# Kernel tuning notes

Hardware: AMD Instinct MI355X
Metric: run time of the kernel (lower is better)

The kernel has to match this reference:

```python
import jax, jax.numpy as jnp
import numpy as np
from jax import lax

N, HW = 64, 240
C0, C1, C2, C3 = 3, 32, 64, 128
HEAD = 1280


def _conv(x, w, stride, pad):
    return lax.conv_general_dilated(
        x, w, (stride, stride), [(pad, pad), (pad, pad)],
        dimension_numbers=("NCHW", "OIHW", "NCHW"))


def _cbr(x, w, alpha, beta, stride, pad, do_relu=True):
    # conv2d with pre-folded BN: y = conv(x,w)*alpha + beta, then ReLU
    y = _conv(x, w, stride, pad)
    y = y * alpha[None, :, None, None] + beta[None, :, None, None]
    return jnp.maximum(y, 0.0) if do_relu else y


def setup_inputs() -> dict:
    key = jax.random.key(0)
    ks = jax.random.split(key, 13)
    f32 = jnp.float32
    inp = {
        "x": jax.random.normal(ks[0], (N, C0, HW, HW), dtype=f32),
        # stem 3x3 s2: 3 -> 32
        "w_stem": jax.random.normal(ks[1], (C1, C0, 3, 3), dtype=f32) * 0.1,
        "a_stem": jax.random.uniform(ks[2], (C1,), dtype=f32, minval=0.5, maxval=1.5),
        "b_stem": jax.random.normal(ks[3], (C1,), dtype=f32) * 0.1,
        # mid 3x3 s2: 32 -> 64
        "w1": jax.random.normal(ks[4], (C2, C1, 3, 3), dtype=f32) * 0.05,
        "a1": jax.random.uniform(ks[5], (C2,), dtype=f32, minval=0.5, maxval=1.5),
        "b1": jax.random.normal(ks[6], (C2,), dtype=f32) * 0.1,
        # pointwise 1x1 s1: 64 -> 128
        "w2": jax.random.normal(ks[7], (C3, C2, 1, 1), dtype=f32) * 0.05,
        "a2": jax.random.uniform(ks[8], (C3,), dtype=f32, minval=0.5, maxval=1.5),
        "b2": jax.random.normal(ks[9], (C3,), dtype=f32) * 0.1,
        # head: GAP + GEMV (w2d [Cout, Cin]) + BN-fold + ReLU
        "w_head": jax.random.normal(ks[10], (HEAD, C3), dtype=f32) * 0.05,
        "a_head": jax.random.uniform(ks[11], (HEAD,), dtype=f32, minval=0.5, maxval=1.5),
        "b_head": jax.random.normal(ks[12], (HEAD,), dtype=f32) * 0.1,
    }
    return inp


def reference(x, w_stem, a_stem, b_stem, w1, a1, b1, w2, a2, b2,
              w_head, a_head, b_head):
    h = _cbr(x, w_stem, a_stem, b_stem, stride=2, pad=1)   # [N,32,120,120]
    h = _cbr(h, w1, a1, b1, stride=2, pad=1)               # [N,64,60,60]
    h = _cbr(h, w2, a2, b2, stride=1, pad=0)               # [N,128,60,60]
    # head: global average pool + GEMV + folded-BN affine + ReLU
    gap = h.mean(axis=(2, 3))                              # [N,128]
    out = jnp.einsum("nc,oc->no", gap, w_head)             # [N,1280]
    out = out * a_head[None, :] + b_head[None, :]
    return jnp.maximum(out, 0.0)
```

## Files before the change

### kernel.cpp

```cpp
#include <hip/hip_runtime.h>

#define N_    64
#define HW_   240
#define H1_   120
#define H2_   60
#define C0_   3
#define C1_   32
#define C2_   64
#define C3_   128
#define HEAD_ 1280

typedef unsigned short US;
typedef short bf16x8 __attribute__((ext_vector_type(8)));
typedef float f32x16 __attribute__((ext_vector_type(16)));

__device__ __forceinline__ US f2bf(float f) {
  union { float f; unsigned u; } v; v.f = f;
  unsigned r = v.u + 0x7FFF + ((v.u >> 16) & 1);
  return (US)(r >> 16);
}

#define H1Q_ROW 3968
#define H1Q_PL  1984

#define ZCHN   368
#define ZTOT   (64 * ZCHN * 4)
__global__ __launch_bounds__(256) void k0_prep(
    const float* __restrict__ w1, const float* __restrict__ w2,
    const float* __restrict__ w0,
    US* __restrict__ h1q, US* __restrict__ wt1, US* __restrict__ wt2,
    US* __restrict__ wt0, float* __restrict__ gap) {
  int gid = blockIdx.x * 256 + threadIdx.x;
  if (gid < ZTOT) {
    int c = gid >> 2, q = gid & 3;
    int n = c / ZCHN, cc = c % ZCHN;
    long off; int y;
    if (cc < 124)      { y = 0;   off = (long)cc * 32; }
    else if (cc < 248) { y = 121; off = (long)(cc - 124) * 32; }
    else               { y = cc - 247; off = H1Q_PL; }
    uint4 z; z.x = z.y = z.z = z.w = 0u;
    *(uint4*)(h1q + ((long)(n * 122 + y)) * H1Q_ROW + off + q * 8) = z;
  } else if (gid < ZTOT + 18432) {
    int e = gid - ZTOT;
    int oc = e / 288, ic = (e / 9) % 32, ky = (e / 3) % 3, kx = e % 3;
    wt1[((ky * 3 + kx) * 64 + oc) * 32 + ic] = f2bf(w1[e]);
  } else if (gid < ZTOT + 18432 + 8192) {
    int e = gid - (ZTOT + 18432);
    wt2[e] = f2bf(w2[e]);
  } else if (gid < ZTOT + 18432 + 8192 + 1024) {
    int e = gid - (ZTOT + 18432 + 8192);
    int oc = e >> 5, k = e & 31;
    wt0[e] = (k < 27) ? f2bf(w0[oc * 27 + k]) : (US)0;
  } else if (gid < ZTOT + 18432 + 8192 + 1024 + 8192) {
    gap[gid - (ZTOT + 18432 + 8192 + 1024)] = 0.f;
  }
}

#define XSW 248
__global__ __launch_bounds__(256) void k1_mfma(
    const float* __restrict__ x, const US* __restrict__ wt0,
    const float* __restrict__ alpha, const float* __restrict__ beta,
    US* __restrict__ h1q) {
  __shared__ float xs[3 * 3 * XSW];
  __shared__ US ot[128 * 32];
  int y = blockIdx.x, n = blockIdx.y;
  int iy0 = 2 * y - 1;
  const float* xn = x + (long)n * C0_ * HW_ * HW_;
  for (int e = threadIdx.x; e < 540; e += 256) {
    int m = e % 60, seg = e / 60;
    int ic = seg / 3, r = seg % 3;
    int iy = iy0 + r;
    float4 v; v.x = v.y = v.z = v.w = 0.f;
    if (iy >= 0) v = *(const float4*)(xn + (long)ic * HW_ * HW_ + iy * HW_ + 4 * m);
    *(float4*)(xs + seg * XSW + 4 + 4 * m) = v;
  }
  if (threadIdx.x < 18) {
    int seg = threadIdx.x >> 1, end = threadIdx.x & 1;
    float4 z; z.x = z.y = z.z = z.w = 0.f;
    *(float4*)(xs + seg * XSW + (end ? 244 : 0)) = z;
  }
  __syncthreads();

  int t = threadIdx.x, wv = t >> 6, l = t & 63;
  int lane31 = l & 31, half = l >> 5;
  int ox = wv * 32 + lane31;
  int oxc = ox < H1_ ? ox : (H1_ - 1);

  float fa[16];
#pragma unroll
  for (int m = 0; m < 2; m++)
#pragma unroll
    for (int j = 0; j < 8; j++) {
      int k = m * 16 + half * 8 + j;
      float v = 0.f;
      if (k < 27) {
        int ic = k / 9, rem = k - ic * 9;
        int ky = rem / 3, kx = rem - ky * 3;
        v = xs[(ic * 3 + ky) * XSW + 3 + 2 * oxc + kx];
      }
      fa[m * 8 + j] = v;
    }
  bf16x8 a0, a1;
#pragma unroll
  for (int j = 0; j < 8; j++) {
    a0[j] = (short)f2bf(fa[j]);
    a1[j] = (short)f2bf(fa[8 + j]);
  }
  const US* wb = wt0 + lane31 * 32 + half * 8;
  bf16x8 b0 = *(const bf16x8*)(wb);
  bf16x8 b1 = *(const bf16x8*)(wb + 16);

  f32x16 acc;
#pragma unroll
  for (int i = 0; i < 16; i++) acc[i] = 0.f;
  acc = __builtin_amdgcn_mfma_f32_32x32x16_bf16(a0, b0, acc, 0, 0, 0);
  acc = __builtin_amdgcn_mfma_f32_32x32x16_bf16(a1, b1, acc, 0, 0, 0);

  int oc = lane31;
  float al = alpha[oc], be = beta[oc];
#pragma unroll
  for (int r = 0; r < 16; r++) {
    int row = (r & 3) + 8 * (r >> 2) + 4 * half;
    float v = fmaxf(fmaf(acc[r], al, be), 0.f);
    ot[(wv * 32 + row) * 32 + oc] = f2bf(v);
  }
  __syncthreads();

  long rowb = ((long)(n * 122 + y + 1)) * H1Q_ROW;
  for (int u = t; u < 480; u += 256) {
    int px = u >> 2, q = u & 3;
    int pl = px & 1;
    int m = (px + 1) >> 1;
    long addr = rowb + (pl ? H1Q_PL : 0) + (long)m * 32 + q * 8;
    *(uint4*)(h1q + addr) = *(const uint4*)(ot + px * 32 + q * 8);
  }
}

#define TS 72
__device__ __forceinline__ void gld_lds16(const void* g, void* l) {
  __builtin_amdgcn_global_load_lds(
      (const __attribute__((address_space(1))) unsigned int*)g,
      (__attribute__((address_space(3))) unsigned int*)l, 16, 0, 0);
}

__global__ __launch_bounds__(256, 2) void k2_fused(
    const US* __restrict__ h1q, const US* __restrict__ wt1,
    const US* __restrict__ wt2,
    const float* __restrict__ a1, const float* __restrict__ b1,
    const float* __restrict__ a2, const float* __restrict__ b2,
    float* __restrict__ gap) {
  __shared__ __align__(16) US st[6 * 4096];
  __shared__ __align__(16) US tile[64 * TS];
  int t = threadIdx.x, w = t >> 6, l = t & 63;
  int lane31 = l & 31, half = l >> 5;

  int n = 8 * blockIdx.x + (blockIdx.y & 7);
  int bxr = blockIdx.y >> 3;
  int ny = bxr < 4 ? 8 : 7;
  int y0 = bxr < 4 ? bxr * 8 : 32 + (bxr - 4) * 7;

  const char* nb = (const char*)(h1q + (long)(n * 122) * H1Q_ROW);

  int wm = w & 1, wn = w >> 1;
  int oc = wn * 32 + lane31;
  int pt = w & 1, og = w >> 1;
  bf16x8 wA[9][2];
#pragma unroll
  for (int kk = 0; kk < 9; kk++)
#pragma unroll
    for (int c = 0; c < 2; c++)
      wA[kk][c] = *(const bf16x8*)(wt1 + (kk * 64 + oc) * 32 + half * 8 + c * 16);
  bf16x8 wB[2][4];
  float al2[2], be2[2];
#pragma unroll
  for (int nt = 0; nt < 2; nt++) {
    int oc2 = (og * 2 + nt) * 32 + lane31;
#pragma unroll
    for (int c = 0; c < 4; c++)
      wB[nt][c] = *(const bf16x8*)(wt2 + oc2 * 64 + half * 8 + c * 16);
    al2[nt] = a2[oc2]; be2[nt] = b2[oc2];
  }
  float al1 = a1[oc], be1 = b1[oc];

  int px = wm * 32 + lane31;
  int xx = px < 60 ? px : 59;
  int abase = xx * 32 + half * 8;
  int usofs[3][2];
#pragma unroll
  for (int kx = 0; kx < 3; kx++)
#pragma unroll
    for (int c = 0; c < 2; c++) {
      int uo = (kx == 1 ? 0 : (kx == 0 ? 1984 : 2016)) + abase + c * 16;
      usofs[kx][c] = uo ^ (((uo >> 6) & 7) << 3);
    }

#pragma unroll
  for (int i = 0; i < 6; i++) {
    int c = i * 256 + t;
    int rw = c >> 9;
    int b = (c & 511) * 16;
    int sb = b ^ (((b >> 7) & 7) << 4);
    int r = 2 * y0 + rw;
    gld_lds16(nb + (long)r * 7936 + sb, (char*)st + (r % 6) * 8192 + b);
  }
  __syncthreads();

  for (int iy = 0; iy < ny; iy++) {
    int y = y0 + iy;
    if (iy + 1 < ny) {
#pragma unroll
      for (int i = 0; i < 4; i++) {
        int c = i * 256 + t;
        int rw = c >> 9;
        int b = (c & 511) * 16;
        int sb = b ^ (((b >> 7) & 7) << 4);
        int r = 2 * y + 3 + rw;
        gld_lds16(nb + (long)r * 7936 + sb,
                  (char*)st + (r % 6) * 8192 + b);
      }
    }

    f32x16 acc;
#pragma unroll
    for (int i = 0; i < 16; i++) acc[i] = 0.f;
#pragma unroll
    for (int ky = 0; ky < 3; ky++) {
      int r = 2 * y + ky;
      int sb6 = (r % 6) * 4096;
#pragma unroll
      for (int kx = 0; kx < 3; kx++) {
#pragma unroll
        for (int c = 0; c < 2; c++) {
          bf16x8 av = *(const bf16x8*)(st + sb6 + usofs[kx][c]);
          acc = __builtin_amdgcn_mfma_f32_32x32x16_bf16(av, wA[ky * 3 + kx][c],
                                                        acc, 0, 0, 0);
        }
      }
    }
#pragma unroll
    for (int r = 0; r < 16; r++) {
      int row = (r & 3) + 8 * (r >> 2) + 4 * half;
      tile[(wm * 32 + row) * TS + oc] = f2bf(fmaxf(fmaf(acc[r], al1, be1), 0.f));
    }
    __syncthreads();

    const US* ab = tile + (pt * 32 + lane31) * TS + half * 8;
    bf16x8 af[4];
#pragma unroll
    for (int c = 0; c < 4; c++) af[c] = *(const bf16x8*)(ab + c * 16);

#pragma unroll
    for (int nt = 0; nt < 2; nt++) {
      int oc2 = (og * 2 + nt) * 32 + lane31;
      f32x16 acc2;
#pragma unroll
      for (int i = 0; i < 16; i++) acc2[i] = 0.f;
#pragma unroll
      for (int c = 0; c < 4; c++)
        acc2 = __builtin_amdgcn_mfma_f32_32x32x16_bf16(af[c], wB[nt][c], acc2,
                                                       0, 0, 0);
      float s = 0.f;
      if (pt == 0) {
#pragma unroll
        for (int r = 0; r < 16; r++) s += fmaxf(fmaf(acc2[r], al2[nt], be2[nt]), 0.f);
      } else {
#pragma unroll
        for (int r = 0; r < 16; r++) {
          int row = (r & 3) + 8 * (r >> 2) + 4 * half;
          if (32 + row < 60) s += fmaxf(fmaf(acc2[r], al2[nt], be2[nt]), 0.f);
        }
      }
      s += __shfl_xor(s, 32);
      if (half == 0) atomicAdd(gap + n * C3_ + oc2, s);
    }
    __syncthreads();
  }
}

__global__ __launch_bounds__(256) void k4_head(
    const float* __restrict__ gap, const float* __restrict__ wh,
    const float* __restrict__ alpha, const float* __restrict__ beta,
    float* __restrict__ out) {
  __shared__ float g[8 * C3_];
  int n0 = blockIdx.y * 8;
  int t = threadIdx.x;
  for (int e = t; e < 8 * C3_; e += 256)
    g[e] = gap[n0 * C3_ + e] * (1.f / 3600.f);
  __syncthreads();
  int o = blockIdx.x * 256 + t;
  const float* wr = wh + (long)o * C3_;
  float acc[8];
#pragma unroll
  for (int i = 0; i < 8; i++) acc[i] = 0.f;
#pragma unroll 4
  for (int c = 0; c < C3_; c += 4) {
    float4 wv = *(const float4*)(wr + c);
#pragma unroll
    for (int i = 0; i < 8; i++) {
      const float* gi = g + i * C3_ + c;
      acc[i] = fmaf(wv.x, gi[0], acc[i]);
      acc[i] = fmaf(wv.y, gi[1], acc[i]);
      acc[i] = fmaf(wv.z, gi[2], acc[i]);
      acc[i] = fmaf(wv.w, gi[3], acc[i]);
    }
  }
  float al = alpha[o], be = beta[o];
#pragma unroll
  for (int i = 0; i < 8; i++)
    out[(n0 + i) * HEAD_ + o] = fmaxf(fmaf(acc[i], al, be), 0.f);
}

extern "C" void kernel_launch(void* const* d_in, const int* in_sizes, int n_in,
                              void* d_out, int out_size, void* d_ws,
                              size_t ws_size, hipStream_t stream) {
  const float* x      = (const float*)d_in[0];
  const float* w_stem = (const float*)d_in[1];
  const float* a_stem = (const float*)d_in[2];
  const float* b_stem = (const float*)d_in[3];
  const float* w1     = (const float*)d_in[4];
  const float* a1     = (const float*)d_in[5];
  const float* b1     = (const float*)d_in[6];
  const float* w2     = (const float*)d_in[7];
  const float* a2     = (const float*)d_in[8];
  const float* b2     = (const float*)d_in[9];
  const float* wh     = (const float*)d_in[10];
  const float* ah     = (const float*)d_in[11];
  const float* bh     = (const float*)d_in[12];
  float* out = (float*)d_out;

  US* h1q = (US*)d_ws;
  US* wt1 = h1q + (size_t)N_ * 122 * H1Q_ROW;
  US* wt2 = wt1 + 9 * 64 * 32;
  US* wt0 = wt2 + C3_ * C2_;
  float* gap = (float*)(wt0 + 1024);

  {
    int total = ZTOT + 18432 + 8192 + 1024 + 8192;
    k0_prep<<<(total + 255) / 256, 256, 0, stream>>>(w1, w2, w_stem, h1q,
                                                     wt1, wt2, wt0, gap);
  }
  {
    dim3 grid(H1_, N_);
    k1_mfma<<<grid, 256, 0, stream>>>(x, wt0, a_stem, b_stem, h1q);
  }
  {
    dim3 grid(8, N_);
    k2_fused<<<grid, 256, 0, stream>>>(h1q, wt1, wt2, a1, b1, a2, b2, gap);
  }
  {
    dim3 grid(HEAD_ / 256, 8);
    k4_head<<<grid, 256, 0, stream>>>(gap, wh, ah, bh, out);
  }
}
```

Baseline: 153.0 us.

## Fuse stem convolution into the fused mid/pointwise kernel via LDS ring buffers

Removes the separate stem kernel and its bf16 intermediate buffer in global memory. Each block of the fused kernel now streams raw input rows into a 6-row LDS ring, computes the stem conv with MFMA directly into the swizzled h1 ring consumed by the 3x3 conv, and overlaps the next rows' stem work with the pointwise stage. This saves the global write and re-read of the 120x120x32 activation and one launch, and no longer needs the zero-fill of padding. In exchange, stem rows on block boundaries are recomputed, LDS use per block grows, and the stem work is serialized inside each block's row loop.

Result: slower. 167.8 us (+9.6%).

```diff
diff --git a/kernel.cpp b/kernel.cpp
--- a/kernel.cpp
+++ b/kernel.cpp
@@ -20,72 +20,43 @@
   return (US)(r >> 16);
 }
 
-#define H1Q_ROW 3968
-#define H1Q_PL  1984
-
-#define ZCHN   368
-#define ZTOT   (64 * ZCHN * 4)
 __global__ __launch_bounds__(256) void k0_prep(
     const float* __restrict__ w1, const float* __restrict__ w2,
     const float* __restrict__ w0,
-    US* __restrict__ h1q, US* __restrict__ wt1, US* __restrict__ wt2,
+    US* __restrict__ wt1, US* __restrict__ wt2,
     US* __restrict__ wt0, float* __restrict__ gap) {
   int gid = blockIdx.x * 256 + threadIdx.x;
-  if (gid < ZTOT) {
-    int c = gid >> 2, q = gid & 3;
-    int n = c / ZCHN, cc = c % ZCHN;
-    long off; int y;
-    if (cc < 124)      { y = 0;   off = (long)cc * 32; }
-    else if (cc < 248) { y = 121; off = (long)(cc - 124) * 32; }
-    else               { y = cc - 247; off = H1Q_PL; }
-    uint4 z; z.x = z.y = z.z = z.w = 0u;
-    *(uint4*)(h1q + ((long)(n * 122 + y)) * H1Q_ROW + off + q * 8) = z;
-  } else if (gid < ZTOT + 18432) {
-    int e = gid - ZTOT;
+  if (gid < 18432) {
+    int e = gid;
     int oc = e / 288, ic = (e / 9) % 32, ky = (e / 3) % 3, kx = e % 3;
     wt1[((ky * 3 + kx) * 64 + oc) * 32 + ic] = f2bf(w1[e]);
-  } else if (gid < ZTOT + 18432 + 8192) {
-    int e = gid - (ZTOT + 18432);
+  } else if (gid < 18432 + 8192) {
+    int e = gid - 18432;
     wt2[e] = f2bf(w2[e]);
-  } else if (gid < ZTOT + 18432 + 8192 + 1024) {
-    int e = gid - (ZTOT + 18432 + 8192);
+  } else if (gid < 18432 + 8192 + 1024) {
+    int e = gid - (18432 + 8192);
     int oc = e >> 5, k = e & 31;
     wt0[e] = (k < 27) ? f2bf(w0[oc * 27 + k]) : (US)0;
-  } else if (gid < ZTOT + 18432 + 8192 + 1024 + 8192) {
-    gap[gid - (ZTOT + 18432 + 8192 + 1024)] = 0.f;
-  }
-}
-
-#define XSW 248
-__global__ __launch_bounds__(256) void k1_mfma(
-    const float* __restrict__ x, const US* __restrict__ wt0,
-    const float* __restrict__ alpha, const float* __restrict__ beta,
-    US* __restrict__ h1q) {
-  __shared__ float xs[3 * 3 * XSW];
-  __shared__ US ot[128 * 32];
-  int y = blockIdx.x, n = blockIdx.y;
-  int iy0 = 2 * y - 1;
-  const float* xn = x + (long)n * C0_ * HW_ * HW_;
-  for (int e = threadIdx.x; e < 540; e += 256) {
-    int m = e % 60, seg = e / 60;
-    int ic = seg / 3, r = seg % 3;
-    int iy = iy0 + r;
-    float4 v; v.x = v.y = v.z = v.w = 0.f;
-    if (iy >= 0) v = *(const float4*)(xn + (long)ic * HW_ * HW_ + iy * HW_ + 4 * m);
-    *(float4*)(xs + seg * XSW + 4 + 4 * m) = v;
-  }
-  if (threadIdx.x < 18) {
-    int seg = threadIdx.x >> 1, end = threadIdx.x & 1;
-    float4 z; z.x = z.y = z.z = z.w = 0.f;
-    *(float4*)(xs + seg * XSW + (end ? 244 : 0)) = z;
-  }
-  __syncthreads();
-
-  int t = threadIdx.x, wv = t >> 6, l = t & 63;
-  int lane31 = l & 31, half = l >> 5;
-  int ox = wv * 32 + lane31;
-  int oxc = ox < H1_ ? ox : (H1_ - 1);
-
+  } else if (gid < 18432 + 8192 + 1024 + 8192) {
+    gap[gid - (18432 + 8192 + 1024)] = 0.f;
+  }
+}
+
+#define TS 72
+__device__ __forceinline__ void gld_lds16(const void* g, void* l) {
+  __builtin_amdgcn_global_load_lds(
+      (const __attribute__((address_space(1))) unsigned int*)g,
+      (__attribute__((address_space(3))) unsigned int*)l, 16, 0, 0);
+}
+
+__device__ __forceinline__ void stem_tile(
+    const float* xr, US* st, int gy, int tb, int lane31, int half,
+    bf16x8 sb0, bf16x8 sb1, float al0, float be0) {
+  int px = tb + lane31;
+  int oxc = px < H1_ ? px : (H1_ - 1);
+  int sl[3];
+#pragma unroll
+  for (int ky = 0; ky < 3; ky++) sl[ky] = (2 * gy - 1 + ky + 6) % 6;
   float fa[16];
 #pragma unroll
   for (int m = 0; m < 2; m++)
@@ -96,7 +67,7 @@
       if (k < 27) {
         int ic = k / 9, rem = k - ic * 9;
         int ky = rem / 3, kx = rem - ky * 3;
-        v = xs[(ic * 3 + ky) * XSW + 3 + 2 * oxc + kx];
+        v = xr[sl[ky] * 768 + ic * 256 + 3 + 2 * oxc + kx];
       }
       fa[m * 8 + j] = v;
     }
@@ -106,50 +77,34 @@
     a0[j] = (short)f2bf(fa[j]);
     a1[j] = (short)f2bf(fa[8 + j]);
   }
-  const US* wb = wt0 + lane31 * 32 + half * 8;
-  bf16x8 b0 = *(const bf16x8*)(wb);
-  bf16x8 b1 = *(const bf16x8*)(wb + 16);
-
   f32x16 acc;
 #pragma unroll
   for (int i = 0; i < 16; i++) acc[i] = 0.f;
-  acc = __builtin_amdgcn_mfma_f32_32x32x16_bf16(a0, b0, acc, 0, 0, 0);
-  acc = __builtin_amdgcn_mfma_f32_32x32x16_bf16(a1, b1, acc, 0, 0, 0);
-
-  int oc = lane31;
-  float al = alpha[oc], be = beta[oc];
+  acc = __builtin_amdgcn_mfma_f32_32x32x16_bf16(a0, sb0, acc, 0, 0, 0);
+  acc = __builtin_amdgcn_mfma_f32_32x32x16_bf16(a1, sb1, acc, 0, 0, 0);
+  int r6 = ((gy + 1) % 6) * 4096;
 #pragma unroll
   for (int r = 0; r < 16; r++) {
     int row = (r & 3) + 8 * (r >> 2) + 4 * half;
-    float v = fmaxf(fmaf(acc[r], al, be), 0.f);
-    ot[(wv * 32 + row) * 32 + oc] = f2bf(v);
-  }
-  __syncthreads();
-
-  long rowb = ((long)(n * 122 + y + 1)) * H1Q_ROW;
-  for (int u = t; u < 480; u += 256) {
-    int px = u >> 2, q = u & 3;
-    int pl = px & 1;
-    int m = (px + 1) >> 1;
-    long addr = rowb + (pl ? H1Q_PL : 0) + (long)m * 32 + q * 8;
-    *(uint4*)(h1q + addr) = *(const uint4*)(ot + px * 32 + q * 8);
-  }
-}
-
-#define TS 72
-__device__ __forceinline__ void gld_lds16(const void* g, void* l) {
-  __builtin_amdgcn_global_load_lds(
-      (const __attribute__((address_space(1))) unsigned int*)g,
-      (__attribute__((address_space(3))) unsigned int*)l, 16, 0, 0);
-}
-
-__global__ __launch_bounds__(256, 2) void k2_fused(
-    const US* __restrict__ h1q, const US* __restrict__ wt1,
-    const US* __restrict__ wt2,
+    int pxo = tb + row;
+    if (pxo < H1_) {
+      int pl = pxo & 1, mm = (pxo + 1) >> 1;
+      int uo = pl * 1984 + mm * 32 + lane31;
+      int us = uo ^ (((uo >> 6) & 7) << 3);
+      st[r6 + us] = f2bf(fmaxf(fmaf(acc[r], al0, be0), 0.f));
+    }
+  }
+}
+
+__global__ __launch_bounds__(256, 2) void k12_fused(
+    const float* __restrict__ x, const US* __restrict__ wt0,
+    const US* __restrict__ wt1, const US* __restrict__ wt2,
+    const float* __restrict__ a0p, const float* __restrict__ b0p,
     const float* __restrict__ a1, const float* __restrict__ b1,
     const float* __restrict__ a2, const float* __restrict__ b2,
     float* __restrict__ gap) {
   __shared__ __align__(16) US st[6 * 4096];
+  __shared__ __align__(16) float xr[6 * 768];
   __shared__ __align__(16) US tile[64 * TS];
   int t = threadIdx.x, w = t >> 6, l = t & 63;
   int lane31 = l & 31, half = l >> 5;
@@ -159,11 +114,15 @@
   int ny = bxr < 4 ? 8 : 7;
   int y0 = bxr < 4 ? bxr * 8 : 32 + (bxr - 4) * 7;
 
-  const char* nb = (const char*)(h1q + (long)(n * 122) * H1Q_ROW);
+  const float* xn = x + (long)n * C0_ * HW_ * HW_;
 
   int wm = w & 1, wn = w >> 1;
   int oc = wn * 32 + lane31;
   int pt = w & 1, og = w >> 1;
+  const US* wb = wt0 + lane31 * 32 + half * 8;
+  bf16x8 sb0 = *(const bf16x8*)(wb);
+  bf16x8 sb1 = *(const bf16x8*)(wb + 16);
+  float al0 = a0p[lane31], be0 = b0p[lane31];
   bf16x8 wA[9][2];
 #pragma unroll
   for (int kk = 0; kk < 9; kk++)
@@ -182,8 +141,8 @@
   }
   float al1 = a1[oc], be1 = b1[oc];
 
-  int px = wm * 32 + lane31;
-  int xx = px < 60 ? px : 59;
+  int px2 = wm * 32 + lane31;
+  int xx = px2 < 60 ? px2 : 59;
   int abase = xx * 32 + half * 8;
   int usofs[3][2];
 #pragma unroll
@@ -194,32 +153,74 @@
       usofs[kx][c] = uo ^ (((uo >> 6) & 7) << 3);
     }
 
-#pragma unroll
-  for (int i = 0; i < 6; i++) {
-    int c = i * 256 + t;
-    int rw = c >> 9;
-    int b = (c & 511) * 16;
-    int sb = b ^ (((b >> 7) & 7) << 4);
-    int r = 2 * y0 + rw;
-    gld_lds16(nb + (long)r * 7936 + sb, (char*)st + (r % 6) * 8192 + b);
-  }
-  __syncthreads();
-
-  for (int iy = 0; iy < ny; iy++) {
-    int y = y0 + iy;
-    if (iy + 1 < ny) {
-#pragma unroll
-      for (int i = 0; i < 4; i++) {
+  {
+    uint4 z; z.x = z.y = z.z = z.w = 0u;
+    for (int e = t; e < 4224; e += 256) {
+      if (e < 3072) ((uint4*)st)[e] = z;
+      else          ((uint4*)xr)[e - 3072] = z;
+    }
+  }
+  __syncthreads();
+  {
+    int r0 = 4 * y0 - 3;
+#pragma unroll
+    for (int i = 0; i < 4; i++) {
+      int c = i * 256 + t;
+      if (c < 960) {
+        int rc = c >> 6;
+        int iy = r0 + rc / 3, ic = rc - (rc / 3) * 3;
+        if (iy >= 0 && (t & 63) < 60)
+          gld_lds16((const char*)(xn + (long)ic * HW_ * HW_ + (long)iy * HW_) +
+                        (t & 63) * 16,
+                    (char*)xr + ((iy % 6) * 768 + ic * 256) * 4 + 16 +
+                        (t & 63) * 16);
+      }
+    }
+  }
+  __syncthreads();
+  for (int j = 0; j < 2; j++) {
+    int gy = 2 * y0 - 1 + j;
+    if (gy >= 0)
+      stem_tile(xr, st, gy, w * 32, lane31, half, sb0, sb1, al0, be0);
+  }
+  __syncthreads();
+  {
+    int r0 = 4 * y0 + 2;
+#pragma unroll
+    for (int i = 0; i < 2; i++) {
+      int c = i * 256 + t;
+      if (c < 384) {
+        int rc = c >> 6;
+        int iy = r0 + rc / 3, ic = rc - (rc / 3) * 3;
+        if ((t & 63) < 60)
+          gld_lds16((const char*)(xn + (long)ic * HW_ * HW_ + (long)iy * HW_) +
+                        (t & 63) * 16,
+                    (char*)xr + ((iy % 6) * 768 + ic * 256) * 4 + 16 +
+                        (t & 63) * 16);
+      }
+    }
+  }
+  __syncthreads();
+  stem_tile(xr, st, 2 * y0 + 1, w * 32, lane31, half, sb0, sb1, al0, be0);
+  __syncthreads();
+
+  for (int it = 0; it < ny; ++it) {
+    int y = y0 + it;
+    bool more = (it + 1 < ny);
+    if (more) {
+      int r0 = 4 * y + 4;
+#pragma unroll
+      for (int i = 0; i < 3; i++) {
         int c = i * 256 + t;
-        int rw = c >> 9;
-        int b = (c & 511) * 16;
-        int sb = b ^ (((b >> 7) & 7) << 4);
-        int r = 2 * y + 3 + rw;
-        gld_lds16(nb + (long)r * 7936 + sb,
-                  (char*)st + (r % 6) * 8192 + b);
-      }
-    }
-
+        int rc = c >> 6;
+        int iy = r0 + rc / 3, ic = rc - (rc / 3) * 3;
+        if ((t & 63) < 60)
+          gld_lds16((const char*)(xn + (long)ic * HW_ * HW_ + (long)iy * HW_) +
+                        (t & 63) * 16,
+                    (char*)xr + ((iy % 6) * 768 + ic * 256) * 4 + 16 +
+                        (t & 63) * 16);
+      }
+    }
     f32x16 acc;
 #pragma unroll
     for (int i = 0; i < 16; i++) acc[i] = 0.f;
@@ -244,11 +245,17 @@
     }
     __syncthreads();
 
+    if (more) {
+      int gy = 2 * y + 2 + (w >> 1);
+      int ws = w & 1;
+      stem_tile(xr, st, gy, ws * 32, lane31, half, sb0, sb1, al0, be0);
+      stem_tile(xr, st, gy, 64 + ws * 32, lane31, half, sb0, sb1, al0, be0);
+    }
+
     const US* ab = tile + (pt * 32 + lane31) * TS + half * 8;
     bf16x8 af[4];
 #pragma unroll
     for (int c = 0; c < 4; c++) af[c] = *(const bf16x8*)(ab + c * 16);
-
 #pragma unroll
     for (int nt = 0; nt < 2; nt++) {
       int oc2 = (og * 2 + nt) * 32 + lane31;
@@ -328,24 +335,20 @@
   const float* bh     = (const float*)d_in[12];
   float* out = (float*)d_out;
 
-  US* h1q = (US*)d_ws;
-  US* wt1 = h1q + (size_t)N_ * 122 * H1Q_ROW;
+  US* wt1 = (US*)d_ws;
   US* wt2 = wt1 + 9 * 64 * 32;
   US* wt0 = wt2 + C3_ * C2_;
   float* gap = (float*)(wt0 + 1024);
 
   {
-    int total = ZTOT + 18432 + 8192 + 1024 + 8192;
-    k0_prep<<<(total + 255) / 256, 256, 0, stream>>>(w1, w2, w_stem, h1q,
+    int total = 18432 + 8192 + 1024 + 8192;
+    k0_prep<<<(total + 255) / 256, 256, 0, stream>>>(w1, w2, w_stem,
                                                      wt1, wt2, wt0, gap);
   }
   {
-    dim3 grid(H1_, N_);
-    k1_mfma<<<grid, 256, 0, stream>>>(x, wt0, a_stem, b_stem, h1q);
-  }
-  {
     dim3 grid(8, N_);
-    k2_fused<<<grid, 256, 0, stream>>>(h1q, wt1, wt2, a1, b1, a2, b2, gap);
+    k12_fused<<<grid, 256, 0, stream>>>(x, wt0, wt1, wt2, a_stem, b_stem,
+                                        a1, b1, a2, b2, gap);
   }
   {
     dim3 grid(HEAD_ / 256, 8);
```
